# Performance work log

Hardware: AMD Instinct MI355X
Metric: run time of the kernel (lower is better)

The kernel has to match this reference:

```python
import jax, jax.numpy as jnp
import numpy as np

B, N, FDIM, REL, H = 4, 256, 256, 16, 8
D = FDIM // H


def setup_inputs() -> dict:
    key = jax.random.key(0)
    ks = jax.random.split(key, 10)
    s_f = 1.0 / np.sqrt(FDIM)
    s_kv = 1.0 / np.sqrt(FDIM + REL)
    return {
        "node_features": jax.random.normal(ks[0], (B, N, FDIM), jnp.float32),
        "relative_positions": jax.random.normal(ks[1], (B, N, N, REL), jnp.float32),
        # torch Linear weights stored transposed -> here [in, out]
        "Wq": jax.random.uniform(ks[2], (FDIM, FDIM), jnp.float32, -s_f, s_f),
        "bq": jax.random.uniform(ks[3], (FDIM,), jnp.float32, -s_f, s_f),
        "Wk": jax.random.uniform(ks[4], (FDIM + REL, FDIM), jnp.float32, -s_kv, s_kv),
        "bk": jax.random.uniform(ks[5], (FDIM,), jnp.float32, -s_kv, s_kv),
        "Wv": jax.random.uniform(ks[6], (FDIM + REL, FDIM), jnp.float32, -s_kv, s_kv),
        "bv": jax.random.uniform(ks[7], (FDIM,), jnp.float32, -s_kv, s_kv),
        "Wo": jax.random.uniform(ks[8], (FDIM, FDIM), jnp.float32, -s_f, s_f),
        "bo": jax.random.uniform(ks[9], (FDIM,), jnp.float32, -s_f, s_f),
    }


def reference(node_features, relative_positions, Wq, bq, Wk, bk, Wv, bv, Wo, bo):
    b, n, f = node_features.shape
    # Q: [b, n_i, H, D]
    Q = (node_features @ Wq + bq).reshape(b, n, H, D)
    # per-edge K/V input: [b, i, j, f+rel] where feature part is node j's features
    nf_j = jnp.broadcast_to(node_features[:, None, :, :], (b, n, n, f))
    kv_in = jnp.concatenate([nf_j, relative_positions], axis=-1)
    K = (kv_in @ Wk + bk).reshape(b, n, n, H, D)  # [b, i, j, h, d]
    V = (kv_in @ Wv + bv).reshape(b, n, n, H, D)
    scale = 1.0 / jnp.sqrt(jnp.asarray(D, node_features.dtype))
    scores = jnp.einsum('bihd,bijhd->bhij', Q, K) * scale
    attn = jax.nn.softmax(scores, axis=-1)
    wv = jnp.einsum('bhij,bijhd->bihd', attn, V).reshape(b, n, f)
    return node_features + (wv @ Wo + bo)
```

## Files before the change

kernel.cpp:

```cpp
#include <hip/hip_runtime.h>


#define BB 4
#define NN 256
#define FD 256
#define RL 16
#define NH 8
#define HD 32

typedef __attribute__((ext_vector_type(8))) short bf16x8;
typedef __attribute__((ext_vector_type(4))) float f32x4;

#define OFF_Q    0
#define OFF_KN   (BB*NN*FD)
#define OFF_VN   (OFF_KN + BB*NN*FD/2)
#define OFF_WVB  (OFF_VN + BB*NN*FD/2)
#define OFF_NFB  (OFF_WVB + BB*NN*FD/2)
#define OFF_WT   (OFF_NFB + BB*NN*FD/2)

#define ATP 260
#define RLT 130

static __device__ __forceinline__ unsigned short f2bf(float x) {
  unsigned int u = __float_as_uint(x);
  unsigned int r = (u + 0x7fffu + ((u >> 16) & 1u)) >> 16;
  return (unsigned short)r;
}
static __device__ __forceinline__ float bf2f(unsigned short h) {
  return __uint_as_float(((unsigned int)h) << 16);
}

__global__ __launch_bounds__(256) void k_prep(
    const float* __restrict__ nf,
    const float* __restrict__ Wq, const float* __restrict__ Wk,
    const float* __restrict__ Wv, const float* __restrict__ Wo,
    float* __restrict__ ws) {
  const int tid = threadIdx.x;
  const int sel = blockIdx.y;
  if (sel == 4) {
    unsigned short* nfB = (unsigned short*)(ws + OFF_NFB);
    const int base = blockIdx.x * 16384;
    #pragma unroll 8
    for (int k = 0; k < 64; ++k) {
      const int idx = base + k * 256 + tid;
      nfB[idx] = f2bf(nf[idx]);
    }
    return;
  }
  const float* W = (sel == 0) ? Wq : (sel == 1) ? Wk : (sel == 2) ? Wv : Wo;
  unsigned short* WT = (unsigned short*)(ws + OFF_WT) + sel * FD * FD;
  __shared__ unsigned short t[64][72];
  const int tx = blockIdx.x & 3, ty = blockIdx.x >> 2;
  const int cx = tid & 63, r0 = tid >> 6;
  #pragma unroll
  for (int rr = r0; rr < 64; rr += 4)
    t[rr][cx] = f2bf(W[(ty * 64 + rr) * FD + tx * 64 + cx]);
  __syncthreads();
  #pragma unroll
  for (int rr = r0; rr < 64; rr += 4)
    WT[(tx * 64 + rr) * FD + ty * 64 + cx] = t[cx][rr];
}

__global__ __launch_bounds__(256) void k_proj(
    const float* __restrict__ bq, const float* __restrict__ bk,
    const float* __restrict__ bv, float* __restrict__ ws) {
  const unsigned short* nfB = (const unsigned short*)(ws + OFF_NFB);
  const int mat = blockIdx.y >> 2;
  const int c0 = (blockIdx.y & 3) * 64;
  const int m0 = blockIdx.x * 64 + (threadIdx.x >> 6) * 16;
  const int l = threadIdx.x & 63;
  const unsigned short* WT = (const unsigned short*)(ws + OFF_WT) + mat * FD * FD;
  const int ar = l & 15, kg = l >> 4;
  f32x4 acc[4];
  #pragma unroll
  for (int nt = 0; nt < 4; ++nt) acc[nt] = (f32x4){0.f, 0.f, 0.f, 0.f};
  #pragma unroll
  for (int ks = 0; ks < 8; ++ks) {
    bf16x8 a = *(const bf16x8*)(nfB + (m0 + ar) * FD + ks * 32 + kg * 8);
    #pragma unroll
    for (int nt = 0; nt < 4; ++nt) {
      bf16x8 b = *(const bf16x8*)(WT + (c0 + nt * 16 + ar) * FD + ks * 32 + kg * 8);
      acc[nt] = __builtin_amdgcn_mfma_f32_16x16x32_bf16(a, b, acc[nt], 0, 0, 0);
    }
  }
  if (mat == 0) {
    const float scale = 0.17677669529663687f;
    float* Qo = ws + OFF_Q;
    #pragma unroll
    for (int nt = 0; nt < 4; ++nt) {
      const int cc = c0 + nt * 16 + ar;
      const float bb = bq[cc];
      #pragma unroll
      for (int i = 0; i < 4; ++i)
        Qo[(m0 + kg * 4 + i) * FD + cc] = (acc[nt][i] + bb) * scale;
    }
  } else if (mat == 1) {
    unsigned short* KnT = (unsigned short*)(ws + OFF_KN);
    const int b2 = m0 >> 8, j0 = (m0 & 255) + kg * 4;
    #pragma unroll
    for (int nt = 0; nt < 4; ++nt) {
      const int cc = c0 + nt * 16 + ar;
      const float bb = bk[cc];
      ushort4 v;
      v.x = f2bf(acc[nt][0] + bb); v.y = f2bf(acc[nt][1] + bb);
      v.z = f2bf(acc[nt][2] + bb); v.w = f2bf(acc[nt][3] + bb);
      *(ushort4*)&KnT[((size_t)b2 * FD + cc) * NN + j0] = v;
    }
  } else {
    unsigned short* Vn = (unsigned short*)(ws + OFF_VN);
    const int b2 = m0 >> 8;
    #pragma unroll
    for (int nt = 0; nt < 4; ++nt) {
      const int cc = c0 + nt * 16 + ar;
      const float bb = bv[cc];
      #pragma unroll
      for (int i = 0; i < 4; ++i) {
        const int j = (m0 & 255) + kg * 4 + i;
        Vn[((size_t)b2 * NN + j) * FD + cc] = f2bf(acc[nt][i] + bb);
      }
    }
  }
}

__global__ __launch_bounds__(256, 4) void k_attn10(
    const float* __restrict__ rel,
    const float* __restrict__ Wk,
    const float* __restrict__ Wv,
    float* __restrict__ ws) {
  const float* Q = ws + OFF_Q;
  const unsigned short* KnB = (const unsigned short*)(ws + OFF_KN);
  const unsigned short* VnB = (const unsigned short*)(ws + OFF_VN);

  const int bid = (blockIdx.x & 7) * 64 + (blockIdx.x >> 3);
  const int b  = bid >> 7;
  const int i0 = (bid & 127) * 2;
  const int tid = threadIdx.x;
  const int l = tid & 63, w = tid >> 6;

  __shared__ float q[2][FD];
  __shared__ float qrs[2][NH * RL];
  __shared__ float ar[2][NH * RL];
  __shared__ __align__(16) float at[2 * NH * ATP];
  __shared__ __align__(16) unsigned int rldsT[2 * RL * RLT];
  float* part = (float*)rldsT;

  q[0][tid] = Q[(b * NN + i0) * FD + tid];
  q[1][tid] = Q[(b * NN + i0 + 1) * FD + tid];

  #pragma unroll
  for (int ii = 0; ii < 2; ++ii) {
    const float4* rp = (const float4*)(rel + ((size_t)(b * NN + i0 + ii)) * (NN * RL));
    #pragma unroll
    for (int m = 0; m < 2; ++m) {
      const int t = tid + 256 * m;
      const int jp = t >> 2, q4 = t & 3;
      float4 va = rp[8 * jp + q4];
      float4 vb = rp[8 * jp + 4 + q4];
      unsigned int* base = &rldsT[(ii * RL + 4 * q4) * RLT + jp];
      base[0]       = (unsigned int)f2bf(va.x) | ((unsigned int)f2bf(vb.x) << 16);
      base[RLT]     = (unsigned int)f2bf(va.y) | ((unsigned int)f2bf(vb.y) << 16);
      base[2 * RLT] = (unsigned int)f2bf(va.z) | ((unsigned int)f2bf(vb.z) << 16);
      base[3 * RLT] = (unsigned int)f2bf(va.w) | ((unsigned int)f2bf(vb.w) << 16);
    }
  }

  {
    const int ii = l >> 5, hh = (l >> 4) & 1, r = l & 15;
    const int h = 2 * w + hh;
    const float* wrow = Wk + (FD + r) * FD + h * HD;
    const float* qq = &q[ii][h * HD];
    float a = 0.f;
    #pragma unroll
    for (int d = 0; d < HD; ++d) a += qq[d] * wrow[d];
    qrs[ii][h * RL + r] = a;
  }
  __syncthreads();

  float s[2][2][4];
  #pragma unroll
  for (int ii = 0; ii < 2; ++ii)
    #pragma unroll
    for (int hh = 0; hh < 2; ++hh)
      #pragma unroll
      for (int jj = 0; jj < 4; ++jj) s[ii][hh][jj] = 0.f;
  {
    const ushort4* kp = (const ushort4*)(KnB + ((size_t)b * FD + 64 * w) * NN) + l;
    #pragma unroll 2
    for (int dd = 0; dd < 8; ++dd) {
      float4 qv00 = *(const float4*)&q[0][64 * w + 4 * dd];
      float4 qv01 = *(const float4*)&q[0][64 * w + 32 + 4 * dd];
      float4 qv10 = *(const float4*)&q[1][64 * w + 4 * dd];
      float4 qv11 = *(const float4*)&q[1][64 * w + 32 + 4 * dd];
      #pragma unroll
      for (int e = 0; e < 4; ++e) {
        ushort4 u0 = kp[(4 * dd + e) * (NN / 4)];
        ushort4 u1 = kp[(32 + 4 * dd + e) * (NN / 4)];
        float4 k0 = make_float4(bf2f(u0.x), bf2f(u0.y), bf2f(u0.z), bf2f(u0.w));
        float4 k1 = make_float4(bf2f(u1.x), bf2f(u1.y), bf2f(u1.z), bf2f(u1.w));
        const float a0 = (&qv00.x)[e], a1 = (&qv01.x)[e];
        const float b0 = (&qv10.x)[e], b1 = (&qv11.x)[e];
        s[0][0][0] += a0 * k0.x; s[0][0][1] += a0 * k0.y;
        s[0][0][2] += a0 * k0.z; s[0][0][3] += a0 * k0.w;
        s[1][0][0] += b0 * k0.x; s[1][0][1] += b0 * k0.y;
        s[1][0][2] += b0 * k0.z; s[1][0][3] += b0 * k0.w;
        s[0][1][0] += a1 * k1.x; s[0][1][1] += a1 * k1.y;
        s[0][1][2] += a1 * k1.z; s[0][1][3] += a1 * k1.w;
        s[1][1][0] += b1 * k1.x; s[1][1][1] += b1 * k1.y;
        s[1][1][2] += b1 * k1.z; s[1][1][3] += b1 * k1.w;
      }
    }
  }

  #pragma unroll
  for (int ii = 0; ii < 2; ++ii) {
    #pragma unroll
    for (int r = 0; r < RL; ++r) {
      uint2 u = *(const uint2*)&rldsT[(ii * RL + r) * RLT + 2 * l];
      float r0 = bf2f((unsigned short)(u.x & 0xffffu));
      float r1 = bf2f((unsigned short)(u.x >> 16));
      float r2 = bf2f((unsigned short)(u.y & 0xffffu));
      float r3 = bf2f((unsigned short)(u.y >> 16));
      const float qa = qrs[ii][(2 * w) * RL + r];
      const float qb = qrs[ii][(2 * w + 1) * RL + r];
      s[ii][0][0] += qa * r0; s[ii][0][1] += qa * r1;
      s[ii][0][2] += qa * r2; s[ii][0][3] += qa * r3;
      s[ii][1][0] += qb * r0; s[ii][1][1] += qb * r1;
      s[ii][1][2] += qb * r2; s[ii][1][3] += qb * r3;
    }
  }

  #pragma unroll
  for (int ii = 0; ii < 2; ++ii) {
    #pragma unroll
    for (int hh = 0; hh < 2; ++hh) {
      float v = fmaxf(fmaxf(s[ii][hh][0], s[ii][hh][1]),
                      fmaxf(s[ii][hh][2], s[ii][hh][3]));
      #pragma unroll
      for (int off = 32; off; off >>= 1) v = fmaxf(v, __shfl_xor(v, off));
      float4 p;
      p.x = __expf(s[ii][hh][0] - v); p.y = __expf(s[ii][hh][1] - v);
      p.z = __expf(s[ii][hh][2] - v); p.w = __expf(s[ii][hh][3] - v);
      float sum = p.x + p.y + p.z + p.w;
      #pragma unroll
      for (int off = 32; off; off >>= 1) sum += __shfl_xor(sum, off);
      const float rec = 1.f / sum;
      p.x *= rec; p.y *= rec; p.z *= rec; p.w *= rec;
      *(float4*)&at[(ii * NH + 2 * w + hh) * ATP + 4 * l] = p;
    }
  }

  #pragma unroll
  for (int ii = 0; ii < 2; ++ii) {
    const int r = l & 15, sl = l >> 4;
    const int h = 2 * w + (sl & 1);
    const int jb = (sl >> 1) * 128;
    const float* atp = at + (ii * NH + h) * ATP + jb;
    const unsigned int* rr_ = &rldsT[(ii * RL + r) * RLT + (jb >> 1)];
    float a = 0.f;
    #pragma unroll 8
    for (int u = 0; u < 64; ++u) {
      unsigned int x = rr_[u];
      a += atp[2 * u]     * bf2f((unsigned short)(x & 0xffffu));
      a += atp[2 * u + 1] * bf2f((unsigned short)(x >> 16));
    }
    a += __shfl_xor(a, 32);
    if (l < 32) ar[ii][32 * w + l] = a;
  }
  __syncthreads();

  {
    const int h = l >> 3;
    const ushort4* vp = (const ushort4*)(VnB + (size_t)b * NN * FD) + l;
    const float* ap0 = at + h * ATP + 64 * w;
    const float* ap1 = at + (NH + h) * ATP + 64 * w;
    float4 a0 = make_float4(0,0,0,0), a1 = make_float4(0,0,0,0);
    #pragma unroll 4
    for (int jj = 0; jj < 64; ++jj) {
      ushort4 u = vp[(64 * w + jj) * (FD / 4)];
      float4 v = make_float4(bf2f(u.x), bf2f(u.y), bf2f(u.z), bf2f(u.w));
      float p0 = ap0[jj], p1 = ap1[jj];
      a0.x += p0*v.x; a0.y += p0*v.y; a0.z += p0*v.z; a0.w += p0*v.w;
      a1.x += p1*v.x; a1.y += p1*v.y; a1.z += p1*v.z; a1.w += p1*v.w;
    }
    ((float4*)part)[w * 64 + l]       = a0;
    ((float4*)part)[(4 + w) * 64 + l] = a1;
  }
  __syncthreads();

  {
    const int c = tid, h2 = c >> 5;
    float s0 = part[c] + part[FD + c] + part[2*FD + c] + part[3*FD + c];
    float s1 = part[4*FD + c] + part[5*FD + c] + part[6*FD + c] + part[7*FD + c];
    #pragma unroll
    for (int r = 0; r < RL; ++r) {
      const float wvr = Wv[(FD + r) * FD + c];
      s0 += ar[0][h2 * RL + r] * wvr;
      s1 += ar[1][h2 * RL + r] * wvr;
    }
    unsigned short* wvB = (unsigned short*)(ws + OFF_WVB);
    wvB[(b * NN + i0) * FD + c]     = f2bf(s0);
    wvB[(b * NN + i0 + 1) * FD + c] = f2bf(s1);
  }
}

__global__ __launch_bounds__(256) void k_out10(
    const float* __restrict__ nf, const float* __restrict__ bo,
    float* __restrict__ out, float* __restrict__ ws) {
  const unsigned short* wvB = (const unsigned short*)(ws + OFF_WVB);
  const unsigned short* WoT = (const unsigned short*)(ws + OFF_WT) + 3 * FD * FD;
  const int c0 = blockIdx.y * 64;
  const int m0 = blockIdx.x * 64 + (threadIdx.x >> 6) * 16;
  const int l = threadIdx.x & 63;
  const int ar = l & 15, kg = l >> 4;
  f32x4 acc[4];
  #pragma unroll
  for (int nt = 0; nt < 4; ++nt) acc[nt] = (f32x4){0.f, 0.f, 0.f, 0.f};
  #pragma unroll
  for (int ks = 0; ks < 8; ++ks) {
    bf16x8 a = *(const bf16x8*)(wvB + (m0 + ar) * FD + ks * 32 + kg * 8);
    #pragma unroll
    for (int nt = 0; nt < 4; ++nt) {
      bf16x8 b = *(const bf16x8*)(WoT + (c0 + nt * 16 + ar) * FD + ks * 32 + kg * 8);
      acc[nt] = __builtin_amdgcn_mfma_f32_16x16x32_bf16(a, b, acc[nt], 0, 0, 0);
    }
  }
  #pragma unroll
  for (int nt = 0; nt < 4; ++nt) {
    const int cc = c0 + nt * 16 + ar;
    const float bb = bo[cc];
    #pragma unroll
    for (int i = 0; i < 4; ++i) {
      const int m = m0 + kg * 4 + i;
      out[m * FD + cc] = nf[m * FD + cc] + acc[nt][i] + bb;
    }
  }
}

extern "C" void kernel_launch(void* const* d_in, const int* in_sizes, int n_in,
                              void* d_out, int out_size, void* d_ws, size_t ws_size,
                              hipStream_t stream) {
  const float* nf  = (const float*)d_in[0];
  const float* rel = (const float*)d_in[1];
  const float* Wq  = (const float*)d_in[2];
  const float* bq  = (const float*)d_in[3];
  const float* Wk  = (const float*)d_in[4];
  const float* bk  = (const float*)d_in[5];
  const float* Wv  = (const float*)d_in[6];
  const float* bv  = (const float*)d_in[7];
  const float* Wo  = (const float*)d_in[8];
  const float* bo  = (const float*)d_in[9];
  float* out = (float*)d_out;
  float* ws  = (float*)d_ws;

  k_prep  <<<dim3(16, 5), 256, 0, stream>>>(nf, Wq, Wk, Wv, Wo, ws);
  k_proj  <<<dim3(16, 12), 256, 0, stream>>>(bq, bk, bv, ws);
  k_attn10<<<512, 256, 0, stream>>>(rel, Wk, Wv, ws);
  k_out10 <<<dim3(16, 4), 256, 0, stream>>>(nf, bo, out, ws);
}
```

Measured before the change: 43.70 us.

## Rewrite attention kernel with MFMA scores, PV, and fused output projection

Replaces the scalar-FMA attention kernel with a 512-thread kernel that handles four query rows per block. It computes QK scores, the relative-position reduction and the PV product with bf16 MFMA instructions, and folds the output projection into the same kernel, so the separate output launch disappears. Q and K are stored row-major in bf16 and V is stored transposed to suit the new fragment layouts. In exchange, MFMA tiles are mostly wasted (only 4 of 16 rows are useful), more intermediates are rounded to bf16, and larger shared memory may limit occupancy.

```diff
diff --git a/kernel.cpp b/kernel.cpp
--- a/kernel.cpp
+++ b/kernel.cpp
@@ -7,19 +7,16 @@
 #define RL 16
 #define NH 8
 #define HD 32
+#define QI 4
 
 typedef __attribute__((ext_vector_type(8))) short bf16x8;
 typedef __attribute__((ext_vector_type(4))) float f32x4;
 
-#define OFF_Q    0
-#define OFF_KN   (BB*NN*FD)
-#define OFF_VN   (OFF_KN + BB*NN*FD/2)
-#define OFF_WVB  (OFF_VN + BB*NN*FD/2)
-#define OFF_NFB  (OFF_WVB + BB*NN*FD/2)
-#define OFF_WT   (OFF_NFB + BB*NN*FD/2)
-
-#define ATP 260
-#define RLT 130
+#define OFF_QB   0
+#define OFF_KNA  131072
+#define OFF_VNT  262144
+#define OFF_NFB  393216
+#define OFF_WT   524288
 
 static __device__ __forceinline__ unsigned short f2bf(float x) {
   unsigned int u = __float_as_uint(x);
@@ -85,253 +82,256 @@
   }
   if (mat == 0) {
     const float scale = 0.17677669529663687f;
-    float* Qo = ws + OFF_Q;
+    unsigned short* Qb = (unsigned short*)(ws + OFF_QB);
     #pragma unroll
     for (int nt = 0; nt < 4; ++nt) {
       const int cc = c0 + nt * 16 + ar;
       const float bb = bq[cc];
       #pragma unroll
       for (int i = 0; i < 4; ++i)
-        Qo[(m0 + kg * 4 + i) * FD + cc] = (acc[nt][i] + bb) * scale;
+        Qb[(m0 + kg * 4 + i) * FD + cc] = f2bf((acc[nt][i] + bb) * scale);
     }
   } else if (mat == 1) {
-    unsigned short* KnT = (unsigned short*)(ws + OFF_KN);
-    const int b2 = m0 >> 8, j0 = (m0 & 255) + kg * 4;
+    unsigned short* Kn = (unsigned short*)(ws + OFF_KNA);
     #pragma unroll
     for (int nt = 0; nt < 4; ++nt) {
       const int cc = c0 + nt * 16 + ar;
       const float bb = bk[cc];
+      #pragma unroll
+      for (int i = 0; i < 4; ++i)
+        Kn[(m0 + kg * 4 + i) * FD + cc] = f2bf(acc[nt][i] + bb);
+    }
+  } else {
+    unsigned short* VnT = (unsigned short*)(ws + OFF_VNT);
+    const int b2 = m0 >> 8, j0 = (m0 & 255) + kg * 4;
+    #pragma unroll
+    for (int nt = 0; nt < 4; ++nt) {
+      const int cc = c0 + nt * 16 + ar;
+      const float bb = bv[cc];
       ushort4 v;
       v.x = f2bf(acc[nt][0] + bb); v.y = f2bf(acc[nt][1] + bb);
       v.z = f2bf(acc[nt][2] + bb); v.w = f2bf(acc[nt][3] + bb);
-      *(ushort4*)&KnT[((size_t)b2 * FD + cc) * NN + j0] = v;
-    }
-  } else {
-    unsigned short* Vn = (unsigned short*)(ws + OFF_VN);
-    const int b2 = m0 >> 8;
-    #pragma unroll
-    for (int nt = 0; nt < 4; ++nt) {
-      const int cc = c0 + nt * 16 + ar;
-      const float bb = bv[cc];
-      #pragma unroll
-      for (int i = 0; i < 4; ++i) {
-        const int j = (m0 & 255) + kg * 4 + i;
-        Vn[((size_t)b2 * NN + j) * FD + cc] = f2bf(acc[nt][i] + bb);
-      }
-    }
-  }
-}
-
-__global__ __launch_bounds__(256, 4) void k_attn10(
+      *(ushort4*)&VnT[((size_t)b2 * FD + cc) * NN + j0] = v;
+    }
+  }
+}
+
+__global__ __launch_bounds__(512, 2) void k_attn11(
     const float* __restrict__ rel,
     const float* __restrict__ Wk,
     const float* __restrict__ Wv,
+    const float* __restrict__ nf,
+    const float* __restrict__ bo,
+    float* __restrict__ out,
     float* __restrict__ ws) {
-  const float* Q = ws + OFF_Q;
-  const unsigned short* KnB = (const unsigned short*)(ws + OFF_KN);
-  const unsigned short* VnB = (const unsigned short*)(ws + OFF_VN);
-
-  const int bid = (blockIdx.x & 7) * 64 + (blockIdx.x >> 3);
-  const int b  = bid >> 7;
-  const int i0 = (bid & 127) * 2;
+  const unsigned short* QbG = (const unsigned short*)(ws + OFF_QB);
+  const unsigned short* KnG = (const unsigned short*)(ws + OFF_KNA);
+  const unsigned short* VTG = (const unsigned short*)(ws + OFF_VNT);
+  const unsigned short* WoT = (const unsigned short*)(ws + OFF_WT) + 3 * FD * FD;
+
+  const int bid = (blockIdx.x & 7) * 32 + (blockIdx.x >> 3);
+  const int b  = bid >> 6;
+  const int i0 = (bid & 63) * QI;
   const int tid = threadIdx.x;
   const int l = tid & 63, w = tid >> 6;
-
-  __shared__ float q[2][FD];
-  __shared__ float qrs[2][NH * RL];
-  __shared__ float ar[2][NH * RL];
-  __shared__ __align__(16) float at[2 * NH * ATP];
-  __shared__ __align__(16) unsigned int rldsT[2 * RL * RLT];
-  float* part = (float*)rldsT;
-
-  q[0][tid] = Q[(b * NN + i0) * FD + tid];
-  q[1][tid] = Q[(b * NN + i0 + 1) * FD + tid];
-
-  #pragma unroll
-  for (int ii = 0; ii < 2; ++ii) {
-    const float4* rp = (const float4*)(rel + ((size_t)(b * NN + i0 + ii)) * (NN * RL));
-    #pragma unroll
-    for (int m = 0; m < 2; ++m) {
-      const int t = tid + 256 * m;
-      const int jp = t >> 2, q4 = t & 3;
-      float4 va = rp[8 * jp + q4];
-      float4 vb = rp[8 * jp + 4 + q4];
-      unsigned int* base = &rldsT[(ii * RL + 4 * q4) * RLT + jp];
-      base[0]       = (unsigned int)f2bf(va.x) | ((unsigned int)f2bf(vb.x) << 16);
-      base[RLT]     = (unsigned int)f2bf(va.y) | ((unsigned int)f2bf(vb.y) << 16);
-      base[2 * RLT] = (unsigned int)f2bf(va.z) | ((unsigned int)f2bf(vb.z) << 16);
-      base[3 * RLT] = (unsigned int)f2bf(va.w) | ((unsigned int)f2bf(vb.w) << 16);
-    }
-  }
-
-  {
-    const int ii = l >> 5, hh = (l >> 4) & 1, r = l & 15;
-    const int h = 2 * w + hh;
+  const int l15 = l & 15, kg = l >> 4;
+
+  __shared__ unsigned short Qb_l[QI * 264];
+  __shared__ unsigned short relT[QI * 16 * 264];
+  __shared__ unsigned short srelP2[8 * 1064];
+  __shared__ float qr_l[QI * 8 * 16];
+  __shared__ float ar_l[QI * 8 * 16];
+  __shared__ unsigned short wv_l[QI * 264];
+
+  {
+    const int t2 = tid * 2, row = t2 >> 8, col = t2 & 255;
+    *(unsigned int*)&Qb_l[row * 264 + col] =
+        *(const unsigned int*)(QbG + ((size_t)(b * NN + i0 + row)) * FD + col);
+  }
+  #pragma unroll
+  for (int m = 0; m < 2; ++m) {
+    const int p = tid + 512 * m, i = p >> 8, j = p & 255;
+    const float4* rp = (const float4*)(rel + (((size_t)(b * NN + i0 + i)) * NN + j) * RL);
+    #pragma unroll
+    for (int q4 = 0; q4 < 4; ++q4) {
+      float4 v = rp[q4];
+      relT[(i * 16 + q4 * 4 + 0) * 264 + j] = f2bf(v.x);
+      relT[(i * 16 + q4 * 4 + 1) * 264 + j] = f2bf(v.y);
+      relT[(i * 16 + q4 * 4 + 2) * 264 + j] = f2bf(v.z);
+      relT[(i * 16 + q4 * 4 + 3) * 264 + j] = f2bf(v.w);
+    }
+  }
+  __syncthreads();
+
+  {
+    const int i = tid >> 7, h = (tid >> 4) & 7, r = tid & 15;
+    const unsigned int* qp = (const unsigned int*)&Qb_l[i * 264 + h * 32];
     const float* wrow = Wk + (FD + r) * FD + h * HD;
-    const float* qq = &q[ii][h * HD];
-    float a = 0.f;
-    #pragma unroll
-    for (int d = 0; d < HD; ++d) a += qq[d] * wrow[d];
-    qrs[ii][h * RL + r] = a;
-  }
-  __syncthreads();
-
-  float s[2][2][4];
-  #pragma unroll
-  for (int ii = 0; ii < 2; ++ii)
-    #pragma unroll
-    for (int hh = 0; hh < 2; ++hh)
-      #pragma unroll
-      for (int jj = 0; jj < 4; ++jj) s[ii][hh][jj] = 0.f;
-  {
-    const ushort4* kp = (const ushort4*)(KnB + ((size_t)b * FD + 64 * w) * NN) + l;
-    #pragma unroll 2
-    for (int dd = 0; dd < 8; ++dd) {
-      float4 qv00 = *(const float4*)&q[0][64 * w + 4 * dd];
-      float4 qv01 = *(const float4*)&q[0][64 * w + 32 + 4 * dd];
-      float4 qv10 = *(const float4*)&q[1][64 * w + 4 * dd];
-      float4 qv11 = *(const float4*)&q[1][64 * w + 32 + 4 * dd];
-      #pragma unroll
-      for (int e = 0; e < 4; ++e) {
-        ushort4 u0 = kp[(4 * dd + e) * (NN / 4)];
-        ushort4 u1 = kp[(32 + 4 * dd + e) * (NN / 4)];
-        float4 k0 = make_float4(bf2f(u0.x), bf2f(u0.y), bf2f(u0.z), bf2f(u0.w));
-        float4 k1 = make_float4(bf2f(u1.x), bf2f(u1.y), bf2f(u1.z), bf2f(u1.w));
-        const float a0 = (&qv00.x)[e], a1 = (&qv01.x)[e];
-        const float b0 = (&qv10.x)[e], b1 = (&qv11.x)[e];
-        s[0][0][0] += a0 * k0.x; s[0][0][1] += a0 * k0.y;
-        s[0][0][2] += a0 * k0.z; s[0][0][3] += a0 * k0.w;
-        s[1][0][0] += b0 * k0.x; s[1][0][1] += b0 * k0.y;
-        s[1][0][2] += b0 * k0.z; s[1][0][3] += b0 * k0.w;
-        s[0][1][0] += a1 * k1.x; s[0][1][1] += a1 * k1.y;
-        s[0][1][2] += a1 * k1.z; s[0][1][3] += a1 * k1.w;
-        s[1][1][0] += b1 * k1.x; s[1][1][1] += b1 * k1.y;
-        s[1][1][2] += b1 * k1.z; s[1][1][3] += b1 * k1.w;
+    float s = 0.f;
+    #pragma unroll
+    for (int d2 = 0; d2 < 16; ++d2) {
+      unsigned int u = qp[d2];
+      s += bf2f((unsigned short)(u & 0xffffu)) * wrow[2 * d2];
+      s += bf2f((unsigned short)(u >> 16)) * wrow[2 * d2 + 1];
+    }
+    qr_l[(i * 8 + h) * 16 + r] = s;
+  }
+  __syncthreads();
+
+  {
+    const int i = w & 3, jh = w >> 2;
+    const int j0 = jh * 128 + l;
+    float rv0[16], rv1[16];
+    #pragma unroll
+    for (int r = 0; r < 16; ++r) {
+      rv0[r] = bf2f(relT[(i * 16 + r) * 264 + j0]);
+      rv1[r] = bf2f(relT[(i * 16 + r) * 264 + j0 + 64]);
+    }
+    #pragma unroll
+    for (int h = 0; h < 8; ++h) {
+      const float* qv = &qr_l[(i * 8 + h) * 16];
+      float s0 = 0.f, s1 = 0.f;
+      #pragma unroll
+      for (int r = 0; r < 16; ++r) { s0 += qv[r] * rv0[r]; s1 += qv[r] * rv1[r]; }
+      srelP2[(i * 8 + h) * 264 + j0]      = f2bf(s0);
+      srelP2[(i * 8 + h) * 264 + j0 + 64] = f2bf(s1);
+    }
+  }
+  __syncthreads();
+
+  const int h = w;
+  f32x4 acc[16];
+  {
+    bf16x8 afrag = *(const bf16x8*)&Qb_l[(l15 & 3) * 264 + h * 32 + kg * 8];
+    #pragma unroll
+    for (int nt = 0; nt < 16; ++nt) {
+      bf16x8 bfrag = *(const bf16x8*)(KnG + ((size_t)(b * NN + nt * 16 + l15)) * FD
+                                      + h * 32 + kg * 8);
+      acc[nt] = __builtin_amdgcn_mfma_f32_16x16x32_bf16(
+          afrag, bfrag, (f32x4){0.f, 0.f, 0.f, 0.f}, 0, 0, 0);
+    }
+    #pragma unroll
+    for (int nt = 0; nt < 16; ++nt) {
+      #pragma unroll
+      for (int ireg = 0; ireg < 4; ++ireg) {
+        const int iC = (kg * 4 + ireg) & 3;
+        acc[nt][ireg] += bf2f(srelP2[(iC * 8 + h) * 264 + nt * 16 + l15]);
       }
     }
   }
-
-  #pragma unroll
-  for (int ii = 0; ii < 2; ++ii) {
-    #pragma unroll
-    for (int r = 0; r < RL; ++r) {
-      uint2 u = *(const uint2*)&rldsT[(ii * RL + r) * RLT + 2 * l];
-      float r0 = bf2f((unsigned short)(u.x & 0xffffu));
-      float r1 = bf2f((unsigned short)(u.x >> 16));
-      float r2 = bf2f((unsigned short)(u.y & 0xffffu));
-      float r3 = bf2f((unsigned short)(u.y >> 16));
-      const float qa = qrs[ii][(2 * w) * RL + r];
-      const float qb = qrs[ii][(2 * w + 1) * RL + r];
-      s[ii][0][0] += qa * r0; s[ii][0][1] += qa * r1;
-      s[ii][0][2] += qa * r2; s[ii][0][3] += qa * r3;
-      s[ii][1][0] += qb * r0; s[ii][1][1] += qb * r1;
-      s[ii][1][2] += qb * r2; s[ii][1][3] += qb * r3;
-    }
-  }
-
-  #pragma unroll
-  for (int ii = 0; ii < 2; ++ii) {
-    #pragma unroll
-    for (int hh = 0; hh < 2; ++hh) {
-      float v = fmaxf(fmaxf(s[ii][hh][0], s[ii][hh][1]),
-                      fmaxf(s[ii][hh][2], s[ii][hh][3]));
-      #pragma unroll
-      for (int off = 32; off; off >>= 1) v = fmaxf(v, __shfl_xor(v, off));
-      float4 p;
-      p.x = __expf(s[ii][hh][0] - v); p.y = __expf(s[ii][hh][1] - v);
-      p.z = __expf(s[ii][hh][2] - v); p.w = __expf(s[ii][hh][3] - v);
-      float sum = p.x + p.y + p.z + p.w;
-      #pragma unroll
-      for (int off = 32; off; off >>= 1) sum += __shfl_xor(sum, off);
-      const float rec = 1.f / sum;
-      p.x *= rec; p.y *= rec; p.z *= rec; p.w *= rec;
-      *(float4*)&at[(ii * NH + 2 * w + hh) * ATP + 4 * l] = p;
-    }
-  }
-
-  #pragma unroll
-  for (int ii = 0; ii < 2; ++ii) {
-    const int r = l & 15, sl = l >> 4;
-    const int h = 2 * w + (sl & 1);
-    const int jb = (sl >> 1) * 128;
-    const float* atp = at + (ii * NH + h) * ATP + jb;
-    const unsigned int* rr_ = &rldsT[(ii * RL + r) * RLT + (jb >> 1)];
-    float a = 0.f;
-    #pragma unroll 8
-    for (int u = 0; u < 64; ++u) {
-      unsigned int x = rr_[u];
-      a += atp[2 * u]     * bf2f((unsigned short)(x & 0xffffu));
-      a += atp[2 * u + 1] * bf2f((unsigned short)(x >> 16));
-    }
-    a += __shfl_xor(a, 32);
-    if (l < 32) ar[ii][32 * w + l] = a;
-  }
-  __syncthreads();
-
-  {
-    const int h = l >> 3;
-    const ushort4* vp = (const ushort4*)(VnB + (size_t)b * NN * FD) + l;
-    const float* ap0 = at + h * ATP + 64 * w;
-    const float* ap1 = at + (NH + h) * ATP + 64 * w;
-    float4 a0 = make_float4(0,0,0,0), a1 = make_float4(0,0,0,0);
-    #pragma unroll 4
-    for (int jj = 0; jj < 64; ++jj) {
-      ushort4 u = vp[(64 * w + jj) * (FD / 4)];
-      float4 v = make_float4(bf2f(u.x), bf2f(u.y), bf2f(u.z), bf2f(u.w));
-      float p0 = ap0[jj], p1 = ap1[jj];
-      a0.x += p0*v.x; a0.y += p0*v.y; a0.z += p0*v.z; a0.w += p0*v.w;
-      a1.x += p1*v.x; a1.y += p1*v.y; a1.z += p1*v.z; a1.w += p1*v.w;
-    }
-    ((float4*)part)[w * 64 + l]       = a0;
-    ((float4*)part)[(4 + w) * 64 + l] = a1;
-  }
-  __syncthreads();
-
-  {
-    const int c = tid, h2 = c >> 5;
-    float s0 = part[c] + part[FD + c] + part[2*FD + c] + part[3*FD + c];
-    float s1 = part[4*FD + c] + part[5*FD + c] + part[6*FD + c] + part[7*FD + c];
-    #pragma unroll
-    for (int r = 0; r < RL; ++r) {
-      const float wvr = Wv[(FD + r) * FD + c];
-      s0 += ar[0][h2 * RL + r] * wvr;
-      s1 += ar[1][h2 * RL + r] * wvr;
-    }
-    unsigned short* wvB = (unsigned short*)(ws + OFF_WVB);
-    wvB[(b * NN + i0) * FD + c]     = f2bf(s0);
-    wvB[(b * NN + i0 + 1) * FD + c] = f2bf(s1);
-  }
-}
-
-__global__ __launch_bounds__(256) void k_out10(
-    const float* __restrict__ nf, const float* __restrict__ bo,
-    float* __restrict__ out, float* __restrict__ ws) {
-  const unsigned short* wvB = (const unsigned short*)(ws + OFF_WVB);
-  const unsigned short* WoT = (const unsigned short*)(ws + OFF_WT) + 3 * FD * FD;
-  const int c0 = blockIdx.y * 64;
-  const int m0 = blockIdx.x * 64 + (threadIdx.x >> 6) * 16;
-  const int l = threadIdx.x & 63;
-  const int ar = l & 15, kg = l >> 4;
-  f32x4 acc[4];
-  #pragma unroll
-  for (int nt = 0; nt < 4; ++nt) acc[nt] = (f32x4){0.f, 0.f, 0.f, 0.f};
-  #pragma unroll
-  for (int ks = 0; ks < 8; ++ks) {
-    bf16x8 a = *(const bf16x8*)(wvB + (m0 + ar) * FD + ks * 32 + kg * 8);
-    #pragma unroll
-    for (int nt = 0; nt < 4; ++nt) {
-      bf16x8 b = *(const bf16x8*)(WoT + (c0 + nt * 16 + ar) * FD + ks * 32 + kg * 8);
-      acc[nt] = __builtin_amdgcn_mfma_f32_16x16x32_bf16(a, b, acc[nt], 0, 0, 0);
-    }
-  }
-  #pragma unroll
-  for (int nt = 0; nt < 4; ++nt) {
-    const int cc = c0 + nt * 16 + ar;
-    const float bb = bo[cc];
-    #pragma unroll
-    for (int i = 0; i < 4; ++i) {
-      const int m = m0 + kg * 4 + i;
-      out[m * FD + cc] = nf[m * FD + cc] + acc[nt][i] + bb;
+  #pragma unroll
+  for (int ireg = 0; ireg < 4; ++ireg) {
+    float mx = acc[0][ireg];
+    #pragma unroll
+    for (int nt = 1; nt < 16; ++nt) mx = fmaxf(mx, acc[nt][ireg]);
+    mx = fmaxf(mx, __shfl_xor(mx, 1)); mx = fmaxf(mx, __shfl_xor(mx, 2));
+    mx = fmaxf(mx, __shfl_xor(mx, 4)); mx = fmaxf(mx, __shfl_xor(mx, 8));
+    float sum = 0.f;
+    #pragma unroll
+    for (int nt = 0; nt < 16; ++nt) {
+      float e = __expf(acc[nt][ireg] - mx);
+      acc[nt][ireg] = e; sum += e;
+    }
+    sum += __shfl_xor(sum, 1); sum += __shfl_xor(sum, 2);
+    sum += __shfl_xor(sum, 4); sum += __shfl_xor(sum, 8);
+    const float rec = 1.f / sum;
+    #pragma unroll
+    for (int nt = 0; nt < 16; ++nt) acc[nt][ireg] *= rec;
+  }
+  __syncthreads();
+
+  if (l < 16) {
+    #pragma unroll
+    for (int nt = 0; nt < 16; ++nt)
+      #pragma unroll
+      for (int ireg = 0; ireg < 4; ++ireg)
+        srelP2[h * 1064 + ireg * 264 + nt * 16 + l] = f2bf(acc[nt][ireg]);
+  }
+  __syncthreads();
+
+  if (w < 4) {
+    const int i = w;
+    const int colh = l15 & 7;
+    f32x4 aa = (f32x4){0.f, 0.f, 0.f, 0.f};
+    #pragma unroll
+    for (int ks = 0; ks < 8; ++ks) {
+      bf16x8 a = *(const bf16x8*)&relT[(i * 16 + l15) * 264 + ks * 32 + kg * 8];
+      bf16x8 bb = *(const bf16x8*)&srelP2[colh * 1064 + i * 264 + ks * 32 + kg * 8];
+      aa = __builtin_amdgcn_mfma_f32_16x16x32_bf16(a, bb, aa, 0, 0, 0);
+    }
+    if (l15 < 8) {
+      #pragma unroll
+      for (int ireg = 0; ireg < 4; ++ireg)
+        ar_l[(i * 8 + l15) * 16 + kg * 4 + ireg] = aa[ireg];
+    }
+  }
+  __syncthreads();
+
+  {
+    const int c = tid & 255, ii0 = tid >> 8, hc = c >> 5;
+    float wvv[16];
+    #pragma unroll
+    for (int r = 0; r < 16; ++r) wvv[r] = Wv[(FD + r) * FD + c];
+    #pragma unroll
+    for (int k2 = 0; k2 < 2; ++k2) {
+      const int i = ii0 + 2 * k2;
+      const float* ap = &ar_l[(i * 8 + hc) * 16];
+      float s = 0.f;
+      #pragma unroll
+      for (int r = 0; r < 16; ++r) s += ap[r] * wvv[r];
+      wv_l[i * 264 + c] = f2bf(s);
+    }
+  }
+  __syncthreads();
+
+  {
+    const int coli = l15 & 3;
+    f32x4 o0 = (f32x4){0.f, 0.f, 0.f, 0.f};
+    f32x4 o1 = (f32x4){0.f, 0.f, 0.f, 0.f};
+    #pragma unroll
+    for (int ks = 0; ks < 8; ++ks) {
+      bf16x8 bb = *(const bf16x8*)&srelP2[h * 1064 + coli * 264 + ks * 32 + kg * 8];
+      bf16x8 a0 = *(const bf16x8*)(VTG + ((size_t)(b * FD + h * 32 + l15)) * NN
+                                   + ks * 32 + kg * 8);
+      bf16x8 a1 = *(const bf16x8*)(VTG + ((size_t)(b * FD + h * 32 + 16 + l15)) * NN
+                                   + ks * 32 + kg * 8);
+      o0 = __builtin_amdgcn_mfma_f32_16x16x32_bf16(a0, bb, o0, 0, 0, 0);
+      o1 = __builtin_amdgcn_mfma_f32_16x16x32_bf16(a1, bb, o1, 0, 0, 0);
+    }
+    if (l15 < 4) {
+      #pragma unroll
+      for (int ireg = 0; ireg < 4; ++ireg) {
+        const int c0_ = h * 32 + kg * 4 + ireg;
+        const int c1_ = c0_ + 16;
+        const int idx0 = l15 * 264 + c0_;
+        const int idx1 = l15 * 264 + c1_;
+        wv_l[idx0] = f2bf(bf2f(wv_l[idx0]) + o0[ireg]);
+        wv_l[idx1] = f2bf(bf2f(wv_l[idx1]) + o1[ireg]);
+      }
+    }
+  }
+  __syncthreads();
+
+  {
+    const int c0_ = w * 32;
+    f32x4 oa0 = (f32x4){0.f, 0.f, 0.f, 0.f};
+    f32x4 oa1 = (f32x4){0.f, 0.f, 0.f, 0.f};
+    #pragma unroll
+    for (int ks = 0; ks < 8; ++ks) {
+      bf16x8 a = *(const bf16x8*)&wv_l[(l15 & 3) * 264 + ks * 32 + kg * 8];
+      bf16x8 b0 = *(const bf16x8*)(WoT + (c0_ + l15) * FD + ks * 32 + kg * 8);
+      bf16x8 b1 = *(const bf16x8*)(WoT + (c0_ + 16 + l15) * FD + ks * 32 + kg * 8);
+      oa0 = __builtin_amdgcn_mfma_f32_16x16x32_bf16(a, b0, oa0, 0, 0, 0);
+      oa1 = __builtin_amdgcn_mfma_f32_16x16x32_bf16(a, b1, oa1, 0, 0, 0);
+    }
+    if (l < 16) {
+      #pragma unroll
+      for (int ireg = 0; ireg < 4; ++ireg) {
+        const int row = (b * NN + i0 + ireg) * FD;
+        const int cc0 = c0_ + l, cc1 = c0_ + 16 + l;
+        out[row + cc0] = nf[row + cc0] + oa0[ireg] + bo[cc0];
+        out[row + cc1] = nf[row + cc1] + oa1[ireg] + bo[cc1];
+      }
     }
   }
 }
@@ -354,6 +354,5 @@
 
   k_prep  <<<dim3(16, 5), 256, 0, stream>>>(nf, Wq, Wk, Wv, Wo, ws);
   k_proj  <<<dim3(16, 12), 256, 0, stream>>>(bq, bk, bv, ws);
-  k_attn10<<<512, 256, 0, stream>>>(rel, Wk, Wv, ws);
-  k_out10 <<<dim3(16, 4), 256, 0, stream>>>(nf, bo, out, ws);
-}
+  k_attn11<<<BB * NN / QI, 512, 0, stream>>>(rel, Wk, Wv, nf, bo, out, ws);
+}
```

Result: faster. 38.27 us (-12.4%).
